# Kernel tuning notes

Hardware: AMD Instinct MI355X
Metric: run time of the kernel (lower is better)

The kernel has to match this reference:

```python
import jax, jax.numpy as jnp
import numpy as np
from functools import partial

IN_DIM = 128
NUM_HEADS = 8
DOWN_DIM = IN_DIM // 2          # 64
HEAD_DIM = DOWN_DIM // NUM_HEADS  # 8
MID = max(1, DOWN_DIM // 16)    # 4 (gate_reduce=16)
DIL = 3
BN_EPS = 1e-5


def conv2d(x, w, padding=0, dilation=1):
    # x: [B,C,H,W], w: [O,I,kh,kw]
    return jax.lax.conv_general_dilated(
        x, w, window_strides=(1, 1),
        padding=[(padding, padding), (padding, padding)],
        rhs_dilation=(dilation, dilation),
        dimension_numbers=("NCHW", "OIHW", "NCHW"))


def batchnorm(x, gamma, beta, mean, var):
    # inference-mode BN over channel dim
    scale = (gamma / jnp.sqrt(var + BN_EPS))[None, :, None, None]
    shift = (beta - mean * gamma / jnp.sqrt(var + BN_EPS))[None, :, None, None]
    return x * scale + shift


def complex_l2_norm(z, eps=1e-6):
    denom = jnp.sqrt(jnp.sum(z.real ** 2 + z.imag ** 2, axis=-1, keepdims=True) + eps)
    return z / denom


def complex_softmax(z):
    return jax.lax.complex(jax.nn.softmax(z.real, axis=-1),
                           jax.nn.softmax(z.imag, axis=-1))


def setup_inputs() -> dict:
    key = jax.random.key(0)
    ks = jax.random.split(key, 6)
    B, H, W = 8, 128, 128
    inp = {}
    inp["x"] = jax.random.normal(ks[0], (B, IN_DIM, H, W), dtype=jnp.float32)
    inp["conv_w"] = jax.random.normal(ks[1], (DOWN_DIM, IN_DIM, 3, 3), dtype=jnp.float32) * 0.02
    inp["bn1_g"] = jnp.ones((DOWN_DIM,), jnp.float32)
    inp["bn1_b"] = jnp.zeros((DOWN_DIM,), jnp.float32)
    inp["bn1_m"] = jnp.zeros((DOWN_DIM,), jnp.float32)
    inp["bn1_v"] = jnp.ones((DOWN_DIM,), jnp.float32)
    inp["cg1_w"] = jax.random.normal(ks[2], (MID, DOWN_DIM, 1, 1), dtype=jnp.float32) * 0.1
    inp["cg1_b"] = jnp.zeros((MID,), jnp.float32)
    inp["cgbn_g"] = jnp.ones((MID,), jnp.float32)
    inp["cgbn_b"] = jnp.zeros((MID,), jnp.float32)
    inp["cgbn_m"] = jnp.zeros((MID,), jnp.float32)
    inp["cgbn_v"] = jnp.ones((MID,), jnp.float32)
    inp["cg2_w"] = jax.random.normal(ks[3], (DOWN_DIM, MID, 1, 1), dtype=jnp.float32) * 0.1
    inp["cg2_b"] = jnp.zeros((DOWN_DIM,), jnp.float32)
    inp["tau"] = jnp.ones((NUM_HEADS, 1, 1), jnp.float32) * (HEAD_DIM ** -0.5)
    return inp


def reference(x, conv_w, bn1_g, bn1_b, bn1_m, bn1_v,
              cg1_w, cg1_b, cgbn_g, cgbn_b, cgbn_m, cgbn_v,
              cg2_w, cg2_b, tau):
    B, C, H, W = x.shape
    # reduce branch: dilated 3x3 conv -> BN -> GELU (exact, matching torch nn.GELU)
    feat = conv2d(x, conv_w, padding=DIL, dilation=DIL)
    feat = batchnorm(feat, bn1_g, bn1_b, bn1_m, bn1_v)
    feat = jax.nn.gelu(feat, approximate=False)

    # q=k=v=g = fft2(feat) (torch computes four identical FFTs; same math)
    F2 = jnp.fft.fft2(feat.astype(jnp.float32), axes=(-2, -1))  # complex64 [B,64,H,W]
    N = H * W
    qkv = F2.reshape(B, NUM_HEADS, HEAD_DIM, N)  # b h d (H W)
    q = complex_l2_norm(qkv)
    k = complex_l2_norm(qkv)
    v = qkv
    # attn: [b,h,d,d] — tiny; contraction over N
    attn = jnp.einsum("bhdn,bhen->bhde", q, jnp.conj(k)) * tau
    attn = complex_softmax(attn)
    out_f = jnp.einsum("bhde,bhen->bhdn", attn, v)
    out_f = out_f.reshape(B, DOWN_DIM, H, W)
    out_f = jnp.abs(jnp.fft.ifft2(out_f, axes=(-2, -1)))

    # gated branch on g = F2
    gr = F2.real
    cg = conv2d(gr, cg1_w) + cg1_b[None, :, None, None]
    cg = batchnorm(cg, cgbn_g, cgbn_b, cgbn_m, cgbn_v)
    cg = jax.nn.gelu(cg, approximate=False)
    cg = conv2d(cg, cg2_w) + cg2_b[None, :, None, None]
    cg = jax.nn.sigmoid(cg)
    gate = cg * F2  # real gate times complex spectrum
    gate = jnp.abs(jnp.fft.ifft2(gate, axes=(-2, -1)))

    y = jnp.concatenate([out_f, gate], axis=1)
    return y + x
```

## Files before the change

kernel.cpp:

```cpp
#include <hip/hip_runtime.h>
#include <hip/hip_bf16.h>
#include <math.h>

#define NB 8
#define CIN 128
#define CDN 64
#define NPIX 16384
#define NHEADS 8
#define HDIM 8

typedef __attribute__((ext_vector_type(8))) short bf16x8;
typedef __attribute__((ext_vector_type(4))) float f32x4;
typedef __attribute__((ext_vector_type(8))) unsigned short u16x8;

struct alignas(8) c2 { float x, y; };

__device__ inline c2 cadd(c2 a, c2 b){ return {a.x+b.x, a.y+b.y}; }
__device__ inline c2 csub(c2 a, c2 b){ return {a.x-b.x, a.y-b.y}; }
__device__ inline c2 cmul(c2 a, c2 b){ return {a.x*b.x - a.y*b.y, a.x*b.y + a.y*b.x}; }
__device__ inline c2 shfl2(c2 v, int m){ return { __shfl_xor(v.x, m, 64), __shfl_xor(v.y, m, 64) }; }
__device__ inline float gelu_exact(float v){ return 0.5f*v*(1.f + erff(v*0.70710678118654752f)); }
__device__ inline unsigned short f2bf(float f){
  __hip_bfloat16 h = __float2bfloat16(f);
  return *reinterpret_cast<unsigned short*>(&h);
}
__device__ inline float bf2f(unsigned short u){ return __uint_as_float((unsigned)u << 16); }

struct Tw { c2 t0; c2 t[6]; };
__device__ inline void tw_init(Tw& w, int t){
  float sn, cs;
  sincosf(-6.283185307179586f * (float)t * (1.f/128.f), &sn, &cs); w.t0 = {cs, sn};
  #pragma unroll
  for (int i = 0; i < 6; ++i) {
    int sp = 32 >> i;
    int j = t & (sp-1);
    sincosf(-3.141592653589793f * (float)j / (float)sp, &sn, &cs);
    w.t[i] = {cs, sn};
  }
}
__device__ inline void fft128_fwd(c2& a, c2& b, int t, const Tw& w){
  c2 s = cadd(a,b), d = csub(a,b);
  a = s; b = cmul(d, w.t0);
  #pragma unroll
  for (int i = 0; i < 6; ++i) {
    int sp = 32 >> i;
    c2 oa = shfl2(a, sp), ob = shfl2(b, sp);
    c2 tw = w.t[i];
    if (t & sp) { a = cmul(csub(oa,a), tw); b = cmul(csub(ob,b), tw); }
    else        { a = cadd(a,oa);           b = cadd(b,ob); }
  }
}
__device__ inline void fft128_inv(c2& a, c2& b, int t, const Tw& w){
  #pragma unroll
  for (int i = 5; i >= 0; --i) {
    int sp = 32 >> i;
    c2 tw = {w.t[i].x, -w.t[i].y};
    c2 oa = shfl2(a, sp), ob = shfl2(b, sp);
    if (t & sp) { a = csub(oa, cmul(a, tw)); b = csub(ob, cmul(b, tw)); }
    else        { a = cadd(a, cmul(oa, tw)); b = cadd(b, cmul(ob, tw)); }
  }
  c2 t0c = {w.t0.x, -w.t0.y};
  c2 wb = cmul(b, t0c);
  b = csub(a, wb);
  a = cadd(a, wb);
}

__device__ inline void gload_lds16(const void* g, void* l){
  __builtin_amdgcn_global_load_lds(
      (const __attribute__((address_space(1))) unsigned int*)g,
      (__attribute__((address_space(3))) unsigned int*)l, 16, 0, 0);
}

__device__ inline int cmapA(int wv, int i){
  if (wv == 0) return i;
  if (wv == 1) return 4 + i;
  if (wv == 2) return i < 2 ? 8 + i : 12 + i;
  if (wv == 3) return 10 + i;
  if (wv < 8) { int a = wv - 4; return i < 2 ? 16 + 2*a + i : 28 - 2*a + i; }
  int a = wv - 8; return i < 2 ? 32 + 2*a + i : 60 - 2*a + i;
}
__device__ inline int cmapB(int wv, int i){
  return i < 2 ? 2*wv + i : 60 - 2*wv + i;
}

__global__ __launch_bounds__(256) void k_prep(const float* __restrict__ x, unsigned short* __restrict__ xT,
                                              const float* __restrict__ w, unsigned short* __restrict__ wP){
  if (blockIdx.x < 512) {
    int b = blockIdx.x >> 6;
    int px = (blockIdx.x & 63)*256 + threadIdx.x;
    const float* xb = x + (size_t)b*CIN*NPIX + px;
    #pragma unroll 2
    for (int ci0 = 0; ci0 < 128; ci0 += 8) {
      u16x8 v;
      #pragma unroll
      for (int j = 0; j < 8; ++j) v[j] = f2bf(xb[(size_t)(ci0+j)*NPIX]);
      int cc = ci0 >> 5;
      *(u16x8*)(xT + (((size_t)(b*4+cc)*NPIX + px)*32 + (ci0 & 31))) = v;
    }
  } else {
    int idx = (blockIdx.x - 512)*256 + threadIdx.x;
    if (idx >= 4*9*64*32) return;
    int cc  = idx / 18432;
    int r   = idx - cc*18432;
    int tap = r / 2048;
    int r2  = r - tap*2048;
    int co  = r2 >> 5;
    int cil = r2 & 31;
    int ci  = cc*32 + cil;
    wP[idx] = f2bf(w[(co*CIN + ci)*9 + tap]);
  }
}

__global__ __launch_bounds__(256) void k_conv(const unsigned short* __restrict__ xT,
    const unsigned short* __restrict__ wP,
    const float* __restrict__ bg, const float* __restrict__ bbeta,
    const float* __restrict__ bm, const float* __restrict__ bv,
    const float* __restrict__ w1,
    unsigned short* __restrict__ feat, float* __restrict__ u){
  __shared__ __align__(16) unsigned short sX[512*32];
  __shared__ float w1s[256];
  const int tid = threadIdx.x;
  const int flat = blockIdx.x + (blockIdx.y << 4) + (blockIdx.z << 7);
  const int half = (flat >> 3) & 1;
  const int tf   = (flat & 7) | ((flat >> 4) << 3);
  const int x0 = (tf & 7) * 16;
  const int y0 = ((tf >> 3) & 7) * 16;
  const int bb = tf >> 6;
  const int coBase = half*32;
  const int wv  = tid >> 6;
  const int l   = tid & 63;
  const int l15 = l & 15;
  const int g   = l >> 4;

  w1s[tid] = w1[tid];

  const bool interior = (x0 >= 16) && (x0 <= 96) && (y0 >= 16) && (y0 <= 96);

  f32x4 acc[2][4];
  #pragma unroll
  for (int m=0;m<2;++m)
    #pragma unroll
    for (int n=0;n<4;++n) acc[m][n] = {0.f,0.f,0.f,0.f};

  const int ko = g*8;

  for (int cc = 0; cc < 4; ++cc) {
    __syncthreads();
    const unsigned short* xcc = xT + ((size_t)(bb*4 + cc))*NPIX*32;
    if (interior) {
      #pragma unroll
      for (int k = 0; k < 8; ++k) {
        int blk = k*4 + wv;
        int idx = blk*64 + l;
        int p = idx >> 2, i = idx & 3;
        int pc = p < 484 ? p : 483;
        int py = pc / 22, px = pc - py*22;
        int gpix = (y0-3+py)*128 + (x0-3+px);
        int sg = i ^ ((p >> 1) & 3);
        const unsigned short* srcp = xcc + (size_t)gpix*32 + sg*8;
        gload_lds16(srcp, (char*)sX + blk*1024);
      }
    } else {
      #pragma unroll
      for (int k = 0; k < 8; ++k) {
        int idx = k*256 + tid;
        int p = idx >> 2, i = idx & 3;
        u16x8 v = {0,0,0,0,0,0,0,0};
        if (p < 484) {
          int py = p / 22, px = p - py*22;
          int gy = y0-3+py, gx = x0-3+px;
          if ((unsigned)gy < 128u && (unsigned)gx < 128u) {
            int sg = i ^ ((p >> 1) & 3);
            v = *(const u16x8*)(xcc + (size_t)(gy*128+gx)*32 + sg*8);
          }
        }
        *(u16x8*)((char*)sX + idx*16) = v;
      }
    }
    __syncthreads();

    const unsigned short* wcc = wP + cc*18432;
    for (int tap = 0; tap < 9; ++tap) {
      int dy = (tap/3)*3, dx = (tap - (tap/3)*3)*3;
      const unsigned short* wt = wcc + tap*2048;
      bf16x8 a[2], b[4];
      #pragma unroll
      for (int m = 0; m < 2; ++m)
        a[m] = *reinterpret_cast<const bf16x8*>(wt + (coBase + m*16 + l15)*32 + ko);
      #pragma unroll
      for (int n = 0; n < 4; ++n) {
        int p = (wv*4 + n + dy)*22 + l15 + dx;
        b[n] = *reinterpret_cast<const bf16x8*>(&sX[p*32 + ((g ^ ((p >> 1) & 3)) << 3)]);
      }
      #pragma unroll
      for (int m = 0; m < 2; ++m)
        #pragma unroll
        for (int n = 0; n < 4; ++n)
          acc[m][n] = __builtin_amdgcn_mfma_f32_16x16x32_bf16(a[m], b[n], acc[m][n], 0, 0, 0);
    }
  }

  float up[4][4];
  #pragma unroll
  for (int n=0;n<4;++n)
    #pragma unroll
    for (int m2=0;m2<4;++m2) up[n][m2] = 0.f;

  #pragma unroll
  for (int m = 0; m < 2; ++m) {
    #pragma unroll
    for (int r = 0; r < 4; ++r) {
      int co = coBase + m*16 + g*4 + r;
      float sc = bg[co] * rsqrtf(bv[co] + 1e-5f);
      float sh = bbeta[co] - bm[co]*sc;
      float wv4[4];
      #pragma unroll
      for (int m2 = 0; m2 < 4; ++m2) wv4[m2] = w1s[m2*64 + co];
      #pragma unroll
      for (int n = 0; n < 4; ++n) {
        int py = wv*4 + n;
        float v = gelu_exact(acc[m][n][r]*sc + sh);
        feat[((size_t)(bb*CDN + co)*128 + (y0+py))*128 + x0 + l15] = f2bf(v);
        #pragma unroll
        for (int m2 = 0; m2 < 4; ++m2) up[n][m2] += wv4[m2]*v;
      }
    }
  }
  #pragma unroll
  for (int n=0;n<4;++n)
    #pragma unroll
    for (int m2=0;m2<4;++m2) {
      up[n][m2] += __shfl_xor(up[n][m2], 16, 64);
      up[n][m2] += __shfl_xor(up[n][m2], 32, 64);
    }
  if (g == 0) {
    #pragma unroll
    for (int n = 0; n < 4; ++n) {
      int py = y0 + wv*4 + n;
      #pragma unroll
      for (int m2 = 0; m2 < 4; ++m2)
        u[((size_t)((bb*2 + half)*4 + m2))*NPIX + py*128 + x0 + l15] = up[n][m2];
    }
  }
}

__global__ __launch_bounds__(256) void k_attn1(const unsigned short* __restrict__ feat, float* __restrict__ part){
  int bh = blockIdx.x, ck = blockIdx.y;
  int b = bh >> 3, h = bh & 7;
  const unsigned short* f = feat + (size_t)(b*CDN + h*HDIM)*NPIX;
  float acc[36];
  #pragma unroll
  for (int i=0;i<36;++i) acc[i]=0.f;
  for (int p = ck*2048 + threadIdx.x; p < (ck+1)*2048; p += 256) {
    float v[8];
    #pragma unroll
    for (int d=0; d<8; ++d) v[d] = bf2f(f[d*NPIX + p]);
    int i = 0;
    #pragma unroll
    for (int d=0; d<8; ++d)
      #pragma unroll
      for (int e=0; e<=d; ++e) acc[i++] += v[d]*v[e];
  }
  #pragma unroll
  for (int i=0;i<36;++i)
    #pragma unroll
    for (int off=32; off; off>>=1) acc[i] += __shfl_xor(acc[i], off, 64);
  __shared__ float red[4][36];
  int wave = threadIdx.x >> 6, lane = threadIdx.x & 63;
  if (lane == 0) {
    #pragma unroll
    for (int i=0;i<36;++i) red[wave][i] = acc[i];
  }
  __syncthreads();
  if (threadIdx.x < 36)
    part[(bh*8+ck)*36 + threadIdx.x] =
      red[0][threadIdx.x]+red[1][threadIdx.x]+red[2][threadIdx.x]+red[3][threadIdx.x];
}

__global__ __launch_bounds__(512) void k_ufft(const float* __restrict__ u,
    const float* __restrict__ b1,
    const float* __restrict__ gg, const float* __restrict__ gbeta,
    const float* __restrict__ gm, const float* __restrict__ gv,
    float* __restrict__ mid){
  __shared__ c2 T[64*129];
  int b = blockIdx.x >> 2, m = blockIdx.x & 3;
  int tid = threadIdx.x, wv = tid >> 6, t = tid & 63;
  Tw w; tw_init(w, t);
  const float* src0 = u + (size_t)((b*2+0)*4+m)*NPIX;
  const float* src1 = u + (size_t)((b*2+1)*4+m)*NPIX;
  c2 ra[16], rb[16];
  #pragma unroll
  for (int i = 0; i < 16; ++i) {
    int y = wv*16 + i;
    ra[i] = {src0[y*128 + t] + src1[y*128 + t], 0.f};
    rb[i] = {src0[y*128 + t + 64] + src1[y*128 + t + 64], 0.f};
  }
  #pragma unroll
  for (int i = 0; i < 16; ++i) fft128_fwd(ra[i], rb[i], t, w);
  c2 ca[16], cb[16];
  if (wv < 4) {
    #pragma unroll
    for (int i = 0; i < 16; ++i) {
      int y = wv*16 + i;
      T[y*129 + t] = ra[i]; T[y*129 + t + 64] = rb[i];
    }
  }
  __syncthreads();
  #pragma unroll
  for (int i = 0; i < 16; ++i) ca[i] = T[t*129 + wv*16 + i];
  __syncthreads();
  if (wv >= 4) {
    #pragma unroll
    for (int i = 0; i < 16; ++i) {
      int y = (wv-4)*16 + i;
      T[y*129 + t] = ra[i]; T[y*129 + t + 64] = rb[i];
    }
  }
  __syncthreads();
  #pragma unroll
  for (int i = 0; i < 16; ++i) cb[i] = T[t*129 + wv*16 + i];
  #pragma unroll
  for (int i = 0; i < 16; ++i) fft128_fwd(ca[i], cb[i], t, w);
  float sc = gg[m]*rsqrtf(gv[m]+1e-5f);
  float sh = gbeta[m] - gm[m]*sc;
  float bb1 = b1[m];
  float* md = mid + (size_t)(b*4+m)*NPIX;
  #pragma unroll
  for (int i = 0; i < 16; ++i) {
    int kx = wv*16 + i;
    md[kx*128 + t]      = gelu_exact((ca[i].x + bb1)*sc + sh);
    md[kx*128 + t + 64] = gelu_exact((cb[i].x + bb1)*sc + sh);
  }
}

__global__ __launch_bounds__(256) void k_gmap(const float* __restrict__ mid, const float* __restrict__ w2,
                                              const float* __restrict__ b2, unsigned* __restrict__ gPack){
  __shared__ float w2s[256], b2s[64];
  w2s[threadIdx.x] = w2[threadIdx.x];
  if (threadIdx.x < 64) b2s[threadIdx.x] = b2[threadIdx.x];
  __syncthreads();
  int b = blockIdx.x >> 6;
  int k = (blockIdx.x & 63)*256 + threadIdx.x;
  const float* md = mid + (size_t)b*4*NPIX + k;
  float m0 = md[0], m1 = md[NPIX], m2 = md[2*NPIX], m3 = md[3*NPIX];
  unsigned* gp = gPack + (size_t)b*32*NPIX + k;
  #pragma unroll 8
  for (int cp = 0; cp < 32; ++cp) {
    float slo = b2s[cp]    + w2s[cp*4]*m0    + w2s[cp*4+1]*m1    + w2s[cp*4+2]*m2    + w2s[cp*4+3]*m3;
    float shi = b2s[cp+32] + w2s[(cp+32)*4]*m0 + w2s[(cp+32)*4+1]*m1 + w2s[(cp+32)*4+2]*m2 + w2s[(cp+32)*4+3]*m3;
    slo = 1.f/(1.f+expf(-slo));
    shi = 1.f/(1.f+expf(-shi));
    gp[(size_t)cp*NPIX] = ((unsigned)f2bf(shi) << 16) | (unsigned)f2bf(slo);
  }
}

__global__ __launch_bounds__(1024)
void k_main(const unsigned short* __restrict__ feat, const unsigned* __restrict__ gPack,
            const float* __restrict__ part, const float* __restrict__ tau,
            const float* __restrict__ x, float* __restrict__ out){
  __shared__ c2 T[128*65];
  int ib = blockIdx.x;
  int tid = threadIdx.x, wv = tid >> 6, t = tid & 63;

  if (ib >= 256) {
    int idx = ib - 256;
    int bh = idx >> 4;
    int b = bh >> 3, h = bh & 7;
    int p = (idx & 15)*1024 + tid;
    float* Af = (float*)T;
    if (tid < 36) {
      float s = 0.f;
      #pragma unroll
      for (int k = 0; k < 8; ++k) s += part[(bh*8+k)*36 + tid];
      Af[64 + tid] = s;
    }
    __syncthreads();
    if (tid == 0) {
      float G[8][8];
      int c2i=0;
      for (int d=0;d<8;++d) for(int e=0;e<=d;++e){
        float s = Af[64 + c2i]; G[d][e]=s; G[e][d]=s; ++c2i;
      }
      float nrm[8];
      for (int d=0;d<8;++d) nrm[d] = sqrtf(16384.f*G[d][d] + 1e-6f);
      float tv = tau[h];
      for (int d=0;d<8;++d) {
        float row[8]; float mx = -1e30f;
        for (int e=0;e<8;++e){ row[e] = tv*16384.f*G[d][e]/(nrm[d]*nrm[e]); mx = fmaxf(mx,row[e]); }
        float s=0.f;
        for (int e=0;e<8;++e){ row[e] = expf(row[e]-mx); s += row[e]; }
        for (int e=0;e<8;++e) Af[d*8+e] = row[e]/s;
      }
    }
    __syncthreads();
    const unsigned short* f = feat + (size_t)(b*CDN + h*HDIM)*NPIX;
    float v[8];
    #pragma unroll
    for (int e=0;e<8;++e) v[e] = bf2f(f[e*NPIX + p]);
    float im = 0.f;
    #pragma unroll
    for (int e=0;e<8;++e) im += v[e];
    im *= 0.125f;
    #pragma unroll
    for (int d=0;d<8;++d){
      float re = 0.f;
      #pragma unroll
      for (int e=0;e<8;++e) re += Af[d*8+e]*v[e];
      size_t o = ((size_t)(b*CIN + h*HDIM + d))*NPIX + p;
      out[o] = sqrtf(re*re + im*im) + x[o];
    }
    return;
  }

  int b = ib >> 5, c = ib & 31;
  Tw w; tw_init(w, t);
  int ta = __brev((64 - (__brev(t) >> 26)) & 63) >> 26;
  const unsigned short* srcA = feat + (size_t)(b*CDN + c)*NPIX;
  const unsigned short* srcB = feat + (size_t)(b*CDN + c + 32)*NPIX;
  const unsigned* gp = gPack + (size_t)(b*32 + c)*NPIX;

  c2 ra[8], rb[8];
  #pragma unroll
  for (int i = 0; i < 8; ++i) {
    int y = wv*8 + i;
    ra[i] = {bf2f(srcA[y*128 + t]),      bf2f(srcB[y*128 + t])};
    rb[i] = {bf2f(srcA[y*128 + t + 64]), bf2f(srcB[y*128 + t + 64])};
  }
  #pragma unroll
  for (int i = 0; i < 8; ++i) fft128_fwd(ra[i], rb[i], t, w);

  #define GUN(w_, lo_, hi_) float lo_ = __uint_as_float((w_) << 16); float hi_ = __uint_as_float((w_) & 0xffff0000u);
  #define CPAIR(I, J) { \
    GUN(gwa[I], g1aI, g2aI); GUN(gwb[I], g1bI, g2bI); \
    GUN(gwa[J], g1aJ, g2aJ); GUN(gwb[J], g1bJ, g2bJ); \
    c2 paI = { __shfl(ca[J].x, ta, 64), -__shfl(ca[J].y, ta, 64) }; \
    c2 paJ = { __shfl(ca[I].x, ta, 64), -__shfl(ca[I].y, ta, 64) }; \
    c2 pbI = { __shfl_xor(cb[J].x, 63, 64), -__shfl_xor(cb[J].y, 63, 64) }; \
    c2 pbJ = { __shfl_xor(cb[I].x, 63, 64), -__shfl_xor(cb[I].y, 63, 64) }; \
    float gsaI=0.5f*(g1aI+g2aI), gdaI=0.5f*(g1aI-g2aI); \
    float gsaJ=0.5f*(g1aJ+g2aJ), gdaJ=0.5f*(g1aJ-g2aJ); \
    float gsbI=0.5f*(g1bI+g2bI), gdbI=0.5f*(g1bI-g2bI); \
    float gsbJ=0.5f*(g1bJ+g2bJ), gdbJ=0.5f*(g1bJ-g2bJ); \
    ca[I] = { gsaI*ca[I].x + gdaI*paI.x, gsaI*ca[I].y + gdaI*paI.y }; \
    ca[J] = { gsaJ*ca[J].x + gdaJ*paJ.x, gsaJ*ca[J].y + gdaJ*paJ.y }; \
    cb[I] = { gsbI*cb[I].x + gdbI*pbI.x, gsbI*cb[I].y + gdbI*pbI.y }; \
    cb[J] = { gsbJ*cb[J].x + gdbJ*pbJ.x, gsbJ*cb[J].y + gdbJ*pbJ.y }; \
  }
  #define CSELF(I) { \
    GUN(gwa[I], g1aI, g2aI); GUN(gwb[I], g1bI, g2bI); \
    c2 paI = { __shfl(ca[I].x, ta, 64), -__shfl(ca[I].y, ta, 64) }; \
    c2 pbI = { __shfl_xor(cb[I].x, 63, 64), -__shfl_xor(cb[I].y, 63, 64) }; \
    float gsaI=0.5f*(g1aI+g2aI), gdaI=0.5f*(g1aI-g2aI); \
    float gsbI=0.5f*(g1bI+g2bI), gdbI=0.5f*(g1bI-g2bI); \
    ca[I] = { gsaI*ca[I].x + gdaI*paI.x, gsaI*ca[I].y + gdaI*paI.y }; \
    cb[I] = { gsbI*cb[I].x + gdbI*pbI.x, gsbI*cb[I].y + gdbI*pbI.y }; \
  }

  #pragma unroll
  for (int i = 0; i < 8; ++i) T[(wv*8 + i)*65 + t] = ra[i];
  __syncthreads();
  {
    int s0 = cmapA(wv,0), s1 = cmapA(wv,1), s2 = cmapA(wv,2), s3 = cmapA(wv,3);
    c2 ca[4], cb[4];
    ca[0]=T[t*65+s0]; ca[1]=T[t*65+s1]; ca[2]=T[t*65+s2]; ca[3]=T[t*65+s3];
    cb[0]=T[(t+64)*65+s0]; cb[1]=T[(t+64)*65+s1]; cb[2]=T[(t+64)*65+s2]; cb[3]=T[(t+64)*65+s3];
    unsigned gwa[4], gwb[4];
    gwa[0]=gp[s0*128+t]; gwa[1]=gp[s1*128+t]; gwa[2]=gp[s2*128+t]; gwa[3]=gp[s3*128+t];
    gwb[0]=gp[s0*128+64+t]; gwb[1]=gp[s1*128+64+t]; gwb[2]=gp[s2*128+64+t]; gwb[3]=gp[s3*128+64+t];
    #pragma unroll
    for (int j = 0; j < 4; ++j) fft128_fwd(ca[j], cb[j], t, w);
    if (wv == 0) { CSELF(0); CSELF(1); CPAIR(2,3); }
    else         { CPAIR(0,3); CPAIR(1,2); }
    #pragma unroll
    for (int j = 0; j < 4; ++j) fft128_inv(ca[j], cb[j], t, w);
    __syncthreads();
    T[t*65+s0]=ca[0]; T[t*65+s1]=ca[1]; T[t*65+s2]=ca[2]; T[t*65+s3]=ca[3];
    T[(t+64)*65+s0]=cb[0]; T[(t+64)*65+s1]=cb[1]; T[(t+64)*65+s2]=cb[2]; T[(t+64)*65+s3]=cb[3];
  }
  __syncthreads();
  #pragma unroll
  for (int i = 0; i < 8; ++i) ra[i] = T[(wv*8 + i)*65 + t];
  __syncthreads();

  #pragma unroll
  for (int i = 0; i < 8; ++i) T[(wv*8 + i)*65 + t] = rb[i];
  __syncthreads();
  {
    int s0 = cmapB(wv,0), s1 = cmapB(wv,1), s2 = cmapB(wv,2), s3 = cmapB(wv,3);
    c2 ca[4], cb[4];
    ca[0]=T[t*65+s0]; ca[1]=T[t*65+s1]; ca[2]=T[t*65+s2]; ca[3]=T[t*65+s3];
    cb[0]=T[(t+64)*65+s0]; cb[1]=T[(t+64)*65+s1]; cb[2]=T[(t+64)*65+s2]; cb[3]=T[(t+64)*65+s3];
    unsigned gwa[4], gwb[4];
    gwa[0]=gp[(64+s0)*128+t]; gwa[1]=gp[(64+s1)*128+t]; gwa[2]=gp[(64+s2)*128+t]; gwa[3]=gp[(64+s3)*128+t];
    gwb[0]=gp[(64+s0)*128+64+t]; gwb[1]=gp[(64+s1)*128+64+t]; gwb[2]=gp[(64+s2)*128+64+t]; gwb[3]=gp[(64+s3)*128+64+t];
    #pragma unroll
    for (int j = 0; j < 4; ++j) fft128_fwd(ca[j], cb[j], t, w);
    CPAIR(0,3); CPAIR(1,2);
    #pragma unroll
    for (int j = 0; j < 4; ++j) fft128_inv(ca[j], cb[j], t, w);
    __syncthreads();
    T[t*65+s0]=ca[0]; T[t*65+s1]=ca[1]; T[t*65+s2]=ca[2]; T[t*65+s3]=ca[3];
    T[(t+64)*65+s0]=cb[0]; T[(t+64)*65+s1]=cb[1]; T[(t+64)*65+s2]=cb[2]; T[(t+64)*65+s3]=cb[3];
  }
  __syncthreads();
  #pragma unroll
  for (int i = 0; i < 8; ++i) rb[i] = T[(wv*8 + i)*65 + t];
  #undef CPAIR
  #undef CSELF
  #undef GUN

  #pragma unroll
  for (int i = 0; i < 8; ++i) fft128_inv(ra[i], rb[i], t, w);
  const float* xr1 = x + ((size_t)(b*CIN + 64 + c))*NPIX;
  const float* xr2 = x + ((size_t)(b*CIN + 96 + c))*NPIX;
  float* o1 = out + ((size_t)(b*CIN + 64 + c))*NPIX;
  float* o2 = out + ((size_t)(b*CIN + 96 + c))*NPIX;
  const float s = 1.f/16384.f;
  #pragma unroll
  for (int i = 0; i < 8; ++i) {
    int y = wv*8 + i;
    o1[y*128 + t]      = fabsf(ra[i].x)*s + xr1[y*128 + t];
    o1[y*128 + t + 64] = fabsf(rb[i].x)*s + xr1[y*128 + t + 64];
    o2[y*128 + t]      = fabsf(ra[i].y)*s + xr2[y*128 + t];
    o2[y*128 + t + 64] = fabsf(rb[i].y)*s + xr2[y*128 + t + 64];
  }
}

extern "C" void kernel_launch(void* const* d_in, const int* in_sizes, int n_in,
                              void* d_out, int out_size, void* d_ws, size_t ws_size,
                              hipStream_t stream){
  const float* x      = (const float*)d_in[0];
  const float* conv_w = (const float*)d_in[1];
  const float* bn1_g  = (const float*)d_in[2];
  const float* bn1_b  = (const float*)d_in[3];
  const float* bn1_m  = (const float*)d_in[4];
  const float* bn1_v  = (const float*)d_in[5];
  const float* cg1_w  = (const float*)d_in[6];
  const float* cg1_b  = (const float*)d_in[7];
  const float* cgbn_g = (const float*)d_in[8];
  const float* cgbn_b = (const float*)d_in[9];
  const float* cgbn_m = (const float*)d_in[10];
  const float* cgbn_v = (const float*)d_in[11];
  const float* cg2_w  = (const float*)d_in[12];
  const float* cg2_b  = (const float*)d_in[13];
  const float* tau    = (const float*)d_in[14];
  float* out = (float*)d_out;

  char* ws = (char*)d_ws;
  unsigned short* feat  = (unsigned short*)ws;
  unsigned short* xT    = (unsigned short*)(ws + 33554432);
  unsigned*       gPack = (unsigned*)(ws + 33554432);
  float*          u     = (float*)(ws + 67108864);
  float*          mid   = (float*)(ws + 71303168);
  unsigned short* wPack = (unsigned short*)(ws + 73400320);
  float*          part  = (float*)(ws + 73547776);

  k_prep<<<800, 256, 0, stream>>>(x, xT, conv_w, wPack);
  k_conv<<<dim3(16,8,NB), 256, 0, stream>>>(xT, wPack, bn1_g, bn1_b, bn1_m, bn1_v, cg1_w, feat, u);
  k_ufft<<<NB*4, 512, 0, stream>>>(u, cg1_b, cgbn_g, cgbn_b, cgbn_m, cgbn_v, mid);
  k_gmap<<<NB*64, 256, 0, stream>>>(mid, cg2_w, cg2_b, gPack);
  k_attn1<<<dim3(NB*NHEADS, 8), 256, 0, stream>>>(feat, part);
  k_main<<<1280, 1024, 0, stream>>>(feat, gPack, part, tau, x, out);
}
```

Before: 211.1 us.

## Regroup kernels so independent attention work co-runs with gate FFT stages

```diff
diff --git a/kernel.cpp b/kernel.cpp
--- a/kernel.cpp
+++ b/kernel.cpp
@@ -244,47 +244,52 @@
   }
 }
 
-__global__ __launch_bounds__(256) void k_attn1(const unsigned short* __restrict__ feat, float* __restrict__ part){
-  int bh = blockIdx.x, ck = blockIdx.y;
-  int b = bh >> 3, h = bh & 7;
-  const unsigned short* f = feat + (size_t)(b*CDN + h*HDIM)*NPIX;
-  float acc[36];
-  #pragma unroll
-  for (int i=0;i<36;++i) acc[i]=0.f;
-  for (int p = ck*2048 + threadIdx.x; p < (ck+1)*2048; p += 256) {
-    float v[8];
-    #pragma unroll
-    for (int d=0; d<8; ++d) v[d] = bf2f(f[d*NPIX + p]);
-    int i = 0;
-    #pragma unroll
-    for (int d=0; d<8; ++d)
-      #pragma unroll
-      for (int e=0; e<=d; ++e) acc[i++] += v[d]*v[e];
-  }
-  #pragma unroll
-  for (int i=0;i<36;++i)
-    #pragma unroll
-    for (int off=32; off; off>>=1) acc[i] += __shfl_xor(acc[i], off, 64);
-  __shared__ float red[4][36];
-  int wave = threadIdx.x >> 6, lane = threadIdx.x & 63;
-  if (lane == 0) {
-    #pragma unroll
-    for (int i=0;i<36;++i) red[wave][i] = acc[i];
-  }
-  __syncthreads();
-  if (threadIdx.x < 36)
-    part[(bh*8+ck)*36 + threadIdx.x] =
-      red[0][threadIdx.x]+red[1][threadIdx.x]+red[2][threadIdx.x]+red[3][threadIdx.x];
-}
-
-__global__ __launch_bounds__(512) void k_ufft(const float* __restrict__ u,
-    const float* __restrict__ b1,
+__global__ __launch_bounds__(512) void k_mid(const unsigned short* __restrict__ feat, float* __restrict__ part,
+    const float* __restrict__ u, const float* __restrict__ b1,
     const float* __restrict__ gg, const float* __restrict__ gbeta,
     const float* __restrict__ gm, const float* __restrict__ gv,
     float* __restrict__ mid){
   __shared__ c2 T[64*129];
-  int b = blockIdx.x >> 2, m = blockIdx.x & 3;
   int tid = threadIdx.x, wv = tid >> 6, t = tid & 63;
+
+  if (blockIdx.x < 512) {
+    int bh = blockIdx.x >> 3, ck = blockIdx.x & 7;
+    int b = bh >> 3, h = bh & 7;
+    const unsigned short* f = feat + (size_t)(b*CDN + h*HDIM)*NPIX;
+    float acc[36];
+    #pragma unroll
+    for (int i=0;i<36;++i) acc[i]=0.f;
+    for (int p = ck*2048 + tid; p < (ck+1)*2048; p += 512) {
+      float v[8];
+      #pragma unroll
+      for (int d=0; d<8; ++d) v[d] = bf2f(f[d*NPIX + p]);
+      int i = 0;
+      #pragma unroll
+      for (int d=0; d<8; ++d)
+        #pragma unroll
+        for (int e=0; e<=d; ++e) acc[i++] += v[d]*v[e];
+    }
+    #pragma unroll
+    for (int i=0;i<36;++i)
+      #pragma unroll
+      for (int off=32; off; off>>=1) acc[i] += __shfl_xor(acc[i], off, 64);
+    float* red = (float*)T;
+    if (t == 0) {
+      #pragma unroll
+      for (int i=0;i<36;++i) red[wv*36 + i] = acc[i];
+    }
+    __syncthreads();
+    if (tid < 36) {
+      float s = 0.f;
+      #pragma unroll
+      for (int k = 0; k < 8; ++k) s += red[k*36 + tid];
+      part[(bh*8+ck)*36 + tid] = s;
+    }
+    return;
+  }
+
+  int ib = blockIdx.x - 512;
+  int b = ib >> 2, m = ib & 3;
   Tw w; tw_init(w, t);
   const float* src0 = u + (size_t)((b*2+0)*4+m)*NPIX;
   const float* src1 = u + (size_t)((b*2+1)*4+m)*NPIX;
@@ -333,86 +338,87 @@
   }
 }
 
-__global__ __launch_bounds__(256) void k_gmap(const float* __restrict__ mid, const float* __restrict__ w2,
-                                              const float* __restrict__ b2, unsigned* __restrict__ gPack){
-  __shared__ float w2s[256], b2s[64];
-  w2s[threadIdx.x] = w2[threadIdx.x];
-  if (threadIdx.x < 64) b2s[threadIdx.x] = b2[threadIdx.x];
-  __syncthreads();
-  int b = blockIdx.x >> 6;
-  int k = (blockIdx.x & 63)*256 + threadIdx.x;
-  const float* md = mid + (size_t)b*4*NPIX + k;
-  float m0 = md[0], m1 = md[NPIX], m2 = md[2*NPIX], m3 = md[3*NPIX];
-  unsigned* gp = gPack + (size_t)b*32*NPIX + k;
-  #pragma unroll 8
-  for (int cp = 0; cp < 32; ++cp) {
-    float slo = b2s[cp]    + w2s[cp*4]*m0    + w2s[cp*4+1]*m1    + w2s[cp*4+2]*m2    + w2s[cp*4+3]*m3;
-    float shi = b2s[cp+32] + w2s[(cp+32)*4]*m0 + w2s[(cp+32)*4+1]*m1 + w2s[(cp+32)*4+2]*m2 + w2s[(cp+32)*4+3]*m3;
-    slo = 1.f/(1.f+expf(-slo));
-    shi = 1.f/(1.f+expf(-shi));
-    gp[(size_t)cp*NPIX] = ((unsigned)f2bf(shi) << 16) | (unsigned)f2bf(slo);
+__global__ __launch_bounds__(1024) void k_tail(const float* __restrict__ mid, const float* __restrict__ w2,
+    const float* __restrict__ b2, unsigned* __restrict__ gPack,
+    const unsigned short* __restrict__ feat, const float* __restrict__ part,
+    const float* __restrict__ tau, const float* __restrict__ x, float* __restrict__ out){
+  __shared__ float S[384];
+  int tid = threadIdx.x;
+
+  if (blockIdx.x < 128) {
+    if (tid < 256) S[tid] = w2[tid];
+    else if (tid < 320) S[tid] = b2[tid - 256];
+    __syncthreads();
+    int b = blockIdx.x >> 4;
+    int k = (blockIdx.x & 15)*1024 + tid;
+    const float* md = mid + (size_t)b*4*NPIX + k;
+    float m0 = md[0], m1 = md[NPIX], m2 = md[2*NPIX], m3 = md[3*NPIX];
+    unsigned* gp = gPack + (size_t)b*32*NPIX + k;
+    #pragma unroll 8
+    for (int cp = 0; cp < 32; ++cp) {
+      float slo = S[256+cp]    + S[cp*4]*m0      + S[cp*4+1]*m1      + S[cp*4+2]*m2      + S[cp*4+3]*m3;
+      float shi = S[256+cp+32] + S[(cp+32)*4]*m0 + S[(cp+32)*4+1]*m1 + S[(cp+32)*4+2]*m2 + S[(cp+32)*4+3]*m3;
+      slo = 1.f/(1.f+expf(-slo));
+      shi = 1.f/(1.f+expf(-shi));
+      gp[(size_t)cp*NPIX] = ((unsigned)f2bf(shi) << 16) | (unsigned)f2bf(slo);
+    }
+    return;
+  }
+
+  int idx = blockIdx.x - 128;
+  int bh = idx >> 4;
+  int b = bh >> 3, h = bh & 7;
+  int p = (idx & 15)*1024 + tid;
+  if (tid < 36) {
+    float s = 0.f;
+    #pragma unroll
+    for (int k = 0; k < 8; ++k) s += part[(bh*8+k)*36 + tid];
+    S[64 + tid] = s;
+  }
+  __syncthreads();
+  if (tid == 0) {
+    float G[8][8];
+    int c2i=0;
+    for (int d=0;d<8;++d) for(int e=0;e<=d;++e){
+      float s = S[64 + c2i]; G[d][e]=s; G[e][d]=s; ++c2i;
+    }
+    float nrm[8];
+    for (int d=0;d<8;++d) nrm[d] = sqrtf(16384.f*G[d][d] + 1e-6f);
+    float tv = tau[h];
+    for (int d=0;d<8;++d) {
+      float row[8]; float mx = -1e30f;
+      for (int e=0;e<8;++e){ row[e] = tv*16384.f*G[d][e]/(nrm[d]*nrm[e]); mx = fmaxf(mx,row[e]); }
+      float s=0.f;
+      for (int e=0;e<8;++e){ row[e] = expf(row[e]-mx); s += row[e]; }
+      for (int e=0;e<8;++e) S[d*8+e] = row[e]/s;
+    }
+  }
+  __syncthreads();
+  const unsigned short* f = feat + (size_t)(b*CDN + h*HDIM)*NPIX;
+  float v[8];
+  #pragma unroll
+  for (int e=0;e<8;++e) v[e] = bf2f(f[e*NPIX + p]);
+  float im = 0.f;
+  #pragma unroll
+  for (int e=0;e<8;++e) im += v[e];
+  im *= 0.125f;
+  #pragma unroll
+  for (int d=0;d<8;++d){
+    float re = 0.f;
+    #pragma unroll
+    for (int e=0;e<8;++e) re += S[d*8+e]*v[e];
+    size_t o = ((size_t)(b*CIN + h*HDIM + d))*NPIX + p;
+    out[o] = sqrtf(re*re + im*im) + x[o];
   }
 }
 
 __global__ __launch_bounds__(1024)
-void k_main(const unsigned short* __restrict__ feat, const unsigned* __restrict__ gPack,
-            const float* __restrict__ part, const float* __restrict__ tau,
-            const float* __restrict__ x, float* __restrict__ out){
+void k_fused(const unsigned short* __restrict__ feat, const unsigned* __restrict__ gPack,
+             const float* __restrict__ x, float* __restrict__ out){
   __shared__ c2 T[128*65];
   int ib = blockIdx.x;
+  int b = ib >> 5, c = ib & 31;
   int tid = threadIdx.x, wv = tid >> 6, t = tid & 63;
-
-  if (ib >= 256) {
-    int idx = ib - 256;
-    int bh = idx >> 4;
-    int b = bh >> 3, h = bh & 7;
-    int p = (idx & 15)*1024 + tid;
-    float* Af = (float*)T;
-    if (tid < 36) {
-      float s = 0.f;
-      #pragma unroll
-      for (int k = 0; k < 8; ++k) s += part[(bh*8+k)*36 + tid];
-      Af[64 + tid] = s;
-    }
-    __syncthreads();
-    if (tid == 0) {
-      float G[8][8];
-      int c2i=0;
-      for (int d=0;d<8;++d) for(int e=0;e<=d;++e){
-        float s = Af[64 + c2i]; G[d][e]=s; G[e][d]=s; ++c2i;
-      }
-      float nrm[8];
-      for (int d=0;d<8;++d) nrm[d] = sqrtf(16384.f*G[d][d] + 1e-6f);
-      float tv = tau[h];
-      for (int d=0;d<8;++d) {
-        float row[8]; float mx = -1e30f;
-        for (int e=0;e<8;++e){ row[e] = tv*16384.f*G[d][e]/(nrm[d]*nrm[e]); mx = fmaxf(mx,row[e]); }
-        float s=0.f;
-        for (int e=0;e<8;++e){ row[e] = expf(row[e]-mx); s += row[e]; }
-        for (int e=0;e<8;++e) Af[d*8+e] = row[e]/s;
-      }
-    }
-    __syncthreads();
-    const unsigned short* f = feat + (size_t)(b*CDN + h*HDIM)*NPIX;
-    float v[8];
-    #pragma unroll
-    for (int e=0;e<8;++e) v[e] = bf2f(f[e*NPIX + p]);
-    float im = 0.f;
-    #pragma unroll
-    for (int e=0;e<8;++e) im += v[e];
-    im *= 0.125f;
-    #pragma unroll
-    for (int d=0;d<8;++d){
-      float re = 0.f;
-      #pragma unroll
-      for (int e=0;e<8;++e) re += Af[d*8+e]*v[e];
-      size_t o = ((size_t)(b*CIN + h*HDIM + d))*NPIX + p;
-      out[o] = sqrtf(re*re + im*im) + x[o];
-    }
-    return;
-  }
-
-  int b = ib >> 5, c = ib & 31;
   Tw w; tw_init(w, t);
   int ta = __brev((64 - (__brev(t) >> 26)) & 63) >> 26;
   const unsigned short* srcA = feat + (size_t)(b*CDN + c)*NPIX;
@@ -557,8 +563,7 @@
 
   k_prep<<<800, 256, 0, stream>>>(x, xT, conv_w, wPack);
   k_conv<<<dim3(16,8,NB), 256, 0, stream>>>(xT, wPack, bn1_g, bn1_b, bn1_m, bn1_v, cg1_w, feat, u);
-  k_ufft<<<NB*4, 512, 0, stream>>>(u, cg1_b, cgbn_g, cgbn_b, cgbn_m, cgbn_v, mid);
-  k_gmap<<<NB*64, 256, 0, stream>>>(mid, cg2_w, cg2_b, gPack);
-  k_attn1<<<dim3(NB*NHEADS, 8), 256, 0, stream>>>(feat, part);
-  k_main<<<1280, 1024, 0, stream>>>(feat, gPack, part, tau, x, out);
-}
+  k_mid<<<544, 512, 0, stream>>>(feat, part, u, cg1_b, cgbn_g, cgbn_b, cgbn_m, cgbn_v, mid);
+  k_tail<<<1152, 1024, 0, stream>>>(mid, cg2_w, cg2_b, gPack, feat, part, tau, x, out);
+  k_fused<<<NB*32, 1024, 0, stream>>>(feat, gPack, x, out);
+}
```

New measurement: 199.5 us, median of 4. 5.5% less time.
